# Kernel optimization log

Hardware: AMD Instinct MI355X
Metric: run time of the kernel (lower is better)

The kernel has to match this reference:

```python
import jax, jax.numpy as jnp
import numpy as np

# Module hyperparameters (from init_kwargs)
H, F = 8, 32            # num_heads, attention_filters
RY, RX = 3, 3           # spatial_radius
PH, PW = 2 * RY + 1, 2 * RX + 1
S = PH * PW             # patch_size = 49
HF = H * F


def setup_inputs() -> dict:
    key = jax.random.key(0)
    ks = jax.random.split(key, 6)
    B, Y, X, C = 4, 64, 64, 256
    x = jax.random.normal(ks[0], (B, Y, X, C), jnp.float32)
    # 1x1 conv kernels == dense matrices over the channel dim (no bias)
    Wq = jax.random.normal(ks[1], (C, HF), jnp.float32) / np.sqrt(C)
    Wk = jax.random.normal(ks[2], (C, HF), jnp.float32) / np.sqrt(C)
    Wv = jax.random.normal(ks[3], (C, HF), jnp.float32) / np.sqrt(C)
    Wo = jax.random.normal(ks[4], (HF, C), jnp.float32) / np.sqrt(HF)
    pos_emb = jax.random.normal(ks[5], (S, HF), jnp.float32) * 0.02
    return {"x": x, "Wq": Wq, "Wk": Wk, "Wv": Wv, "Wo": Wo, "pos_emb": pos_emb}


def reference(x, Wq, Wk, Wv, Wo, pos_emb):
    B, Y, X, C = x.shape
    dtype = x.dtype
    # 1x1 conv projections
    Q = x @ Wq                       # (B,Y,X,HF)
    K = x @ Wk
    V = x @ Wv
    # clipped patch centers (borders reuse interior patches)
    cy = jnp.clip(jnp.arange(Y), RY, Y - RY - 1)   # (Y,)
    cx = jnp.clip(jnp.arange(X), RX, X - RX - 1)   # (X,)
    # query relative-position indices within its patch
    qy = jnp.arange(Y) - cy + RY
    qx = jnp.arange(X) - cx + RX
    qidx = qy[:, None] * PW + qx[None, :]          # (Y,X) in [0,S)
    Q = Q + pos_emb[qidx]                          # add query pos embedding (HF)
    Q = Q.reshape(B, Y, X, H, F)
    K = K.reshape(B, Y, X, H, F)
    V = V.reshape(B, Y, X, H, F)
    cy_g, cx_g = jnp.meshgrid(cy, cx, indexing="ij")  # (Y,X)
    scale = jnp.asarray(1.0 / np.sqrt(F), dtype)
    NEG = jnp.asarray(-1e9, dtype)
    m = jnp.full((B, Y, X, H, 1), NEG, dtype)      # running max
    l = jnp.zeros((B, Y, X, H, 1), dtype)          # running sum-exp
    acc = jnp.zeros((B, Y, X, H, F), dtype)        # running value accumulator
    dy_vec = np.arange(-RY, RY + 1)                # within-chunk offsets ('col' mode)
    for dx in range(-RX, RX + 1):                  # chunk loop over columns (7 chunks)
        ny = jnp.clip(cy_g[None, :, :] + dy_vec[:, None, None], 0, Y - 1)  # (PH,Y,X)
        nx = jnp.clip(cx_g[None, :, :] + dx, 0, X - 1)                     # (1,Y,X)
        nx = jnp.broadcast_to(nx, ny.shape)
        sidx = (dy_vec + RY) * PW + (dx + RX)      # (PH,) relative-pos indices
        # gather neighbor K/V: (B,PH,Y,X,H,F)
        Kc = K[:, ny, nx] + pos_emb[sidx].reshape(PH, 1, 1, H, F)
        Vc = V[:, ny, nx]
        sc = jnp.einsum("byxhf,bsyxhf->byxhs", Q, Kc) * scale  # (B,Y,X,H,PH)
        new_m = jnp.maximum(m, sc.max(axis=-1, keepdims=True))
        alpha = jnp.exp(m - new_m)
        p = jnp.exp(sc - new_m)
        l = l * alpha + p.sum(axis=-1, keepdims=True)
        acc = acc * alpha + jnp.einsum("byxhs,bsyxhf->byxhf", p, Vc)
        m = new_m
    out = (acc / (l + 1e-8)).reshape(B, Y, X, HF) @ Wo
    return out
```

## Files before the change

kernel.cpp:

```cpp
#include <hip/hip_runtime.h>
#include <hip/hip_bf16.h>

static constexpr int NPOS = 4 * 64 * 64;
static constexpr int CD   = 256;
#define QSCALE (0.17677669529663687f * 1.4426950408889634f)

typedef __attribute__((ext_vector_type(8))) short bf16x8;
typedef __attribute__((ext_vector_type(4))) float f32x4;

__device__ __forceinline__ float bf2f(unsigned short u) {
    return __uint_as_float((unsigned int)u << 16);
}
__device__ __forceinline__ unsigned short bfbits(float f) {
    union { __hip_bfloat16 h; unsigned short u; } cv;
    cv.h = __float2bfloat16(f);
    return cv.u;
}
__device__ __forceinline__ unsigned int packbf2(float lo, float hi) {
    union { __hip_bfloat162 h; unsigned int u; } cv;
    cv.h.x = __float2bfloat16(lo);
    cv.h.y = __float2bfloat16(hi);
    return cv.u;
}
__device__ __forceinline__ uint4 pack8(float4 a, float4 b) {
    uint4 u;
    u.x = packbf2(a.x, a.y); u.y = packbf2(a.z, a.w);
    u.z = packbf2(b.x, b.y); u.w = packbf2(b.z, b.w);
    return u;
}
__device__ __forceinline__ void pl32swap(unsigned &a, unsigned &b) {
    auto r = __builtin_amdgcn_permlane32_swap(a, b, false, false);
    a = r[0]; b = r[1];
}
__device__ __forceinline__ void pl16swap(unsigned &a, unsigned &b) {
    auto r = __builtin_amdgcn_permlane16_swap(a, b, false, false);
    a = r[0]; b = r[1];
}

__global__ __launch_bounds__(256) void convert_kernel(
    const float* __restrict__ Wq, const float* __restrict__ Wk,
    const float* __restrict__ Wv, const float* __restrict__ Wo,
    const float* __restrict__ pe,
    __hip_bfloat16* __restrict__ Wfrag,
    __hip_bfloat16* __restrict__ pebf,
    __hip_bfloat16* __restrict__ Wofrag)
{
    int t = blockIdx.x * 256 + threadIdx.x;
    if (t < 24576) {
        int L = t & 63, ng = (t >> 6) & 7, s = (t >> 9) & 7, T = t >> 12;
        int mat = T >> 1;
        const float* src = (mat == 0) ? Wq : (mat == 1) ? Wk : Wv;
        int ncol  = (T & 1) * 128 + ng * 16 + (L & 15);
        int kbase = s * 32 + (L >> 4) * 8;
        __hip_bfloat16* dst = Wfrag + ((size_t)((T * 8 + s) * 8 + ng) * 64 + L) * 8;
#pragma unroll
        for (int j = 0; j < 8; ++j)
            dst[j] = __float2bfloat16(src[(kbase + j) * 256 + ncol]);
    } else if (t < 26624) {
        int u = t - 24576;
        int L = u & 63, Tn = (u >> 6) & 3, h = u >> 8;
        int s = Tn * 16 + (L & 15);
        int kbase = (L >> 4) * 8;
        __hip_bfloat16* dst = pebf + ((size_t)((h * 4 + Tn) * 64 + L)) * 8;
#pragma unroll
        for (int j = 0; j < 8; ++j) {
            float v = (s < 49) ? pe[s * 256 + h * 32 + kbase + j] * QSCALE : 0.f;
            dst[j] = __float2bfloat16(v);
        }
    } else if (t < 34816) {
        int u = t - 26624;
        int L = u & 63, ng = (u >> 6) & 7, s = (u >> 9) & 7, T = (u >> 12) & 1;
        int ncol  = T * 128 + ng * 16 + (L & 15);
        int kbase = s * 32 + (L >> 4) * 8;
        __hip_bfloat16* dst = Wofrag + ((size_t)((T * 8 + s) * 8 + ng) * 64 + L) * 8;
#pragma unroll
        for (int j = 0; j < 8; ++j)
            dst[j] = __float2bfloat16(Wo[(kbase + j) * 256 + ncol]);
    }
}

__global__ __launch_bounds__(256, 4) void qkv_mfma(
    const float* __restrict__ x,
    const __hip_bfloat16* __restrict__ Wfrag,
    const float* __restrict__ pe,
    unsigned short* __restrict__ QA,
    unsigned short* __restrict__ Kd,
    unsigned short* __restrict__ Vt)
{
    __shared__ __align__(16) unsigned short smem[256 * 68];
    short* As0 = (short*)smem;
    short* As1 = As0 + 2048;
    const int t = threadIdx.x;
    const int rowbase = blockIdx.x * 64;
    const int g = blockIdx.y;
    const int L = t & 63;
    const int wave = t >> 6;
    const int quad = L >> 4, lrow = L & 15;
    const int T = g * 2 + (wave >> 1);
    const int ngb = (wave & 1) * 4;

    f32x4 acc[4][4];
#pragma unroll
    for (int i = 0; i < 4; ++i)
#pragma unroll
        for (int j = 0; j < 4; ++j) acc[i][j] = (f32x4){0.f, 0.f, 0.f, 0.f};

    const float* xsrc = x + (size_t)(rowbase + (t >> 2)) * CD + (t & 3) * 8;
    const __hip_bfloat16* wbase = Wfrag + ((size_t)(T * 8 * 8 + ngb) * 64 + L) * 8;

    float4 f0 = ((const float4*)xsrc)[0];
    float4 f1 = ((const float4*)xsrc)[1];
    ((uint4*)As0)[t] = pack8(f0, f1);
    f0 = ((const float4*)(xsrc + 32))[0];
    f1 = ((const float4*)(xsrc + 32))[1];

    bf16x8 bfr[4];
#pragma unroll
    for (int j = 0; j < 4; ++j)
        bfr[j] = *(const bf16x8*)(wbase + (size_t)j * 64 * 8);
    __syncthreads();

#pragma unroll
    for (int s = 0; s < 8; ++s) {
        bf16x8 nbfr[4];
        if (s < 7) {
#pragma unroll
            for (int j = 0; j < 4; ++j)
                nbfr[j] = *(const bf16x8*)(wbase + (size_t)((s + 1) * 8 + j) * 64 * 8);
        }
        if (s < 7) {
            ((uint4*)((s & 1) ? As0 : As1))[t] = pack8(f0, f1);
            if (s < 6) {
                f0 = ((const float4*)(xsrc + (s + 2) * 32))[0];
                f1 = ((const float4*)(xsrc + (s + 2) * 32))[1];
            }
        }
        const short* Ab = (s & 1) ? As1 : As0;
#pragma unroll
        for (int i = 0; i < 4; ++i) {
            bf16x8 af = *(const bf16x8*)(Ab + (i * 16 + lrow) * 32 + quad * 8);
#pragma unroll
            for (int j = 0; j < 4; ++j)
                acc[i][j] = __builtin_amdgcn_mfma_f32_16x16x32_bf16(af, bfr[j], acc[i][j], 0, 0, 0);
        }
        __syncthreads();
#pragma unroll
        for (int j = 0; j < 4; ++j) bfr[j] = nbfr[j];
    }

    if (g == 0) {
#pragma unroll
        for (int i = 0; i < 4; ++i)
#pragma unroll
            for (int r = 0; r < 4; ++r) {
                int row = rowbase + i * 16 + quad * 4 + r;
                int yy = (row >> 6) & 63, xx = row & 63;
                int cy = min(max(yy, 3), 60), cx = min(max(xx, 3), 60);
                int qidx = (yy - cy + 3) * 7 + (xx - cx + 3);
#pragma unroll
                for (int j = 0; j < 4; ++j) {
                    int c = wave * 64 + j * 16 + lrow;
                    QA[(size_t)row * CD + c] = bfbits(acc[i][j][r] + pe[qidx * 256 + c]);
                }
            }
    } else if (g == 1) {
#pragma unroll
        for (int i = 0; i < 4; ++i)
#pragma unroll
            for (int r = 0; r < 4; ++r) {
                int row = rowbase + i * 16 + quad * 4 + r;
#pragma unroll
                for (int j = 0; j < 4; ++j) {
                    int c = wave * 64 + j * 16 + lrow;
                    Kd[(size_t)row * CD + c] = bfbits(acc[i][j][r] * QSCALE);
                }
            }
    } else {
        unsigned short* vt = smem;
#pragma unroll
        for (int i = 0; i < 4; ++i)
#pragma unroll
            for (int j = 0; j < 4; ++j) {
                int c = wave * 64 + j * 16 + lrow;
                int row0 = i * 16 + quad * 4;
                *(unsigned int*)&vt[c * 68 + row0] =
                    (unsigned int)bfbits(acc[i][j][0]) | ((unsigned int)bfbits(acc[i][j][1]) << 16);
                *(unsigned int*)&vt[c * 68 + row0 + 2] =
                    (unsigned int)bfbits(acc[i][j][2]) | ((unsigned int)bfbits(acc[i][j][3]) << 16);
            }
        __syncthreads();
        const int grp = t >> 4, lig = t & 15;
        const int row_off = lig * 4;
#pragma unroll
        for (int pass = 0; pass < 16; ++pass) {
            int c = pass * 16 + grp;
            *(ushort4*)(Vt + (size_t)c * 16384 + rowbase + row_off) =
                *(const ushort4*)&vt[c * 68 + row_off];
        }
    }
}

__global__ __launch_bounds__(512) void attn_oproj(
    const unsigned short* __restrict__ QA,
    const unsigned short* __restrict__ Kd,
    const unsigned short* __restrict__ Vt,
    const __hip_bfloat16* __restrict__ pebf,
    const __hip_bfloat16* __restrict__ Wofrag,
    float* __restrict__ out)
{
    __shared__ __align__(16) unsigned short qpes[8][16 * 72];
    __shared__ __align__(16) unsigned short At[16 * 264];
    const int t = threadIdx.x, w = t >> 6, L = t & 63;
    const int lrow = L & 15, quad = L >> 4;
    const int bid = blockIdx.x;
    const int tile = ((bid & 7) << 7) | (bid >> 3);
    const int pos0 = tile * 16;
    const int x0 = pos0 & 63;
    const int yy = (pos0 >> 6) & 63, bb = pos0 >> 12;
    const int cy = min(max(yy, 3), 60);
    const int h = w;

    const int kc0 = min(max(x0 - 8 + lrow, 0), 63);
    const int kc1 = min(max(x0 + 8 + lrow, 0), 63);
    const f32x4 zero = {0.f, 0.f, 0.f, 0.f};
    unsigned short* qp = qpes[w];

    const int cx = min(max(x0 + lrow, 3), 60) - x0 + 5;
    int qiA[4], qiB[4];
    float mkA[4], mkB[4];
#pragma unroll
    for (int r = 0; r < 4; ++r) {
        const int sl = quad * 4 + r;
        int dxa = sl - cx;
        qiA[r] = lrow * 72 + min(max(dxa, 0), 6);
        mkA[r] = ((unsigned)dxa <= 6u) ? 1.f : 0.f;
        int dxb = 16 + sl - cx;
        qiB[r] = lrow * 72 + min(max(dxb, 0), 6);
        mkB[r] = ((unsigned)dxb <= 6u) ? 1.f : 0.f;
    }

    const bf16x8 qa = *(const bf16x8*)(QA + (size_t)(pos0 + lrow) * 256 + h * 32 + quad * 8);

#pragma unroll
    for (int Tn = 0; Tn < 4; ++Tn) {
        bf16x8 bp = *(const bf16x8*)(pebf + ((size_t)((h * 4 + Tn) * 64 + L)) * 8);
        f32x4 c = __builtin_amdgcn_mfma_f32_16x16x32_bf16(bp, qa, zero, 0, 0, 0);
        *(unsigned int*)&qp[lrow * 72 + Tn * 16 + quad * 4]     = packbf2(c[0], c[1]);
        *(unsigned int*)&qp[lrow * 72 + Tn * 16 + quad * 4 + 2] = packbf2(c[2], c[3]);
    }
    __builtin_amdgcn_s_waitcnt(0xc07f);

    float lacc = 0.f;
    f32x4 oT0 = zero, oT1 = zero;
    int rowpos = bb * 4096 + (cy - 3) * 64;

    const size_t koff = h * 32 + quad * 8;
    const size_t voff0 = (size_t)(h * 32 + lrow) * 16384 + x0 - 8 + quad * 8;
    const size_t voff1 = (size_t)(h * 32 + 16 + lrow) * 16384 + x0 - 8 + quad * 8;
    bf16x8 bk0 = *(const bf16x8*)(Kd + (size_t)(rowpos + kc0) * 256 + koff);
    bf16x8 bk1 = *(const bf16x8*)(Kd + (size_t)(rowpos + kc1) * 256 + koff);
    bf16x8 bv0 = *(const bf16x8*)(Vt + voff0 + rowpos);
    bf16x8 bv1 = *(const bf16x8*)(Vt + voff1 + rowpos);

    int qpofs = 0;
    for (int dy = 0; dy < 7; ++dy) {
        const int rnext = rowpos + 64;
        bf16x8 nk0, nk1, nv0, nv1;
        if (dy < 6) {
            nk0 = *(const bf16x8*)(Kd + (size_t)(rnext + kc0) * 256 + koff);
            nk1 = *(const bf16x8*)(Kd + (size_t)(rnext + kc1) * 256 + koff);
            nv0 = *(const bf16x8*)(Vt + voff0 + rnext);
            nv1 = *(const bf16x8*)(Vt + voff1 + rnext);
        }
        f32x4 s0 = __builtin_amdgcn_mfma_f32_16x16x32_bf16(bk0, qa, zero, 0, 0, 0);
        f32x4 s1 = __builtin_amdgcn_mfma_f32_16x16x32_bf16(bk1, qa, zero, 0, 0, 0);
        float e00 = exp2f(s0[0] + bf2f(qp[qiA[0] + qpofs])) * mkA[0];
        float e01 = exp2f(s0[1] + bf2f(qp[qiA[1] + qpofs])) * mkA[1];
        float e02 = exp2f(s0[2] + bf2f(qp[qiA[2] + qpofs])) * mkA[2];
        float e03 = exp2f(s0[3] + bf2f(qp[qiA[3] + qpofs])) * mkA[3];
        float e10 = exp2f(s1[0] + bf2f(qp[qiB[0] + qpofs])) * mkB[0];
        float e11 = exp2f(s1[1] + bf2f(qp[qiB[1] + qpofs])) * mkB[1];
        float e12 = exp2f(s1[2] + bf2f(qp[qiB[2] + qpofs])) * mkB[2];
        float e13 = exp2f(s1[3] + bf2f(qp[qiB[3] + qpofs])) * mkB[3];
        lacc += ((e00 + e01) + (e02 + e03)) + ((e10 + e11) + (e12 + e13));

        unsigned p0 = packbf2(e00, e01), p1 = packbf2(e02, e03);
        unsigned z0 = packbf2(e10, e11), z1 = packbf2(e12, e13);
        pl32swap(p0, z0);
        pl16swap(p0, z0);
        pl32swap(p1, z1);
        pl16swap(p1, z1);
        union { unsigned u[4]; bf16x8 v; } pb;
        pb.u[0] = p0; pb.u[1] = p1; pb.u[2] = z0; pb.u[3] = z1;

        oT0 = __builtin_amdgcn_mfma_f32_16x16x32_bf16(bv0, pb.v, oT0, 0, 0, 0);
        oT1 = __builtin_amdgcn_mfma_f32_16x16x32_bf16(bv1, pb.v, oT1, 0, 0, 0);
        bk0 = nk0; bk1 = nk1; bv0 = nv0; bv1 = nv1;
        rowpos = rnext;
        qpofs += 7;
    }

    lacc += __shfl_xor(lacc, 16);
    lacc += __shfl_xor(lacc, 32);
    const float inv = 1.f / (lacc + 1e-8f);

    {
        const int base = lrow * 264 + h * 32 + quad * 4;
        *(unsigned int*)&At[base]          = packbf2(oT0[0] * inv, oT0[1] * inv);
        *(unsigned int*)&At[base + 2]      = packbf2(oT0[2] * inv, oT0[3] * inv);
        *(unsigned int*)&At[base + 16]     = packbf2(oT1[0] * inv, oT1[1] * inv);
        *(unsigned int*)&At[base + 16 + 2] = packbf2(oT1[2] * inv, oT1[3] * inv);
    }
    __syncthreads();

    const int T = w >> 2;
    const int ngb = (w & 3) * 2;
    f32x4 acc[2];
    acc[0] = zero; acc[1] = zero;

#pragma unroll
    for (int s = 0; s < 8; ++s) {
        bf16x8 bfr[2];
#pragma unroll
        for (int j = 0; j < 2; ++j)
            bfr[j] = *(const bf16x8*)(Wofrag +
                      ((size_t)((T * 8 + s) * 8 + ngb + j) * 64 + L) * 8);
        bf16x8 af = *(const bf16x8*)(At + lrow * 264 + s * 32 + quad * 8);
#pragma unroll
        for (int j = 0; j < 2; ++j)
            acc[j] = __builtin_amdgcn_mfma_f32_16x16x32_bf16(af, bfr[j], acc[j], 0, 0, 0);
    }

#pragma unroll
    for (int r = 0; r < 4; ++r) {
        int row = pos0 + quad * 4 + r;
#pragma unroll
        for (int j = 0; j < 2; ++j) {
            int c = w * 32 + j * 16 + lrow;
            out[(size_t)row * CD + c] = acc[j][r];
        }
    }
}

extern "C" void kernel_launch(void* const* d_in, const int* in_sizes, int n_in,
                              void* d_out, int out_size, void* d_ws, size_t ws_size,
                              hipStream_t stream)
{
    const float* x  = (const float*)d_in[0];
    const float* Wq = (const float*)d_in[1];
    const float* Wk = (const float*)d_in[2];
    const float* Wv = (const float*)d_in[3];
    const float* Wo = (const float*)d_in[4];
    const float* pe = (const float*)d_in[5];
    float* out = (float*)d_out;

    char* ws = (char*)d_ws;
    unsigned short* QA = (unsigned short*)ws;
    unsigned short* Kd = (unsigned short*)(ws + (8u << 20));
    unsigned short* Vt = (unsigned short*)(ws + (16u << 20));
    char* fr = ws + (24u << 20) + 4096;
    __hip_bfloat16* Wfrag  = (__hip_bfloat16*)fr;
    __hip_bfloat16* pebf   = (__hip_bfloat16*)(fr + (384u << 10));
    __hip_bfloat16* Wofrag = (__hip_bfloat16*)(fr + (416u << 10));

    convert_kernel<<<136, 256, 0, stream>>>(Wq, Wk, Wv, Wo, pe, Wfrag, pebf, Wofrag);
    qkv_mfma<<<dim3(256, 3), 256, 0, stream>>>(x, Wfrag, pe, QA, Kd, Vt);
    attn_oproj<<<1024, 512, 0, stream>>>(QA, Kd, Vt, pebf, Wofrag, out);
}
```

Measured before the change: 124.8 us.

## Merge Q/K/V projection blocks to load each x tile once into LDS

The QKV projection kernel used to launch three separate blocks per 64-row tile, one each for Q, K and V. Each of those blocks streamed the same fp32 x rows from global memory through a double-buffered LDS pipeline. Now a single 768-thread block loads the whole 64x256 x tile into LDS as bf16 once and runs twelve waves covering all three projections. This removes the threefold redundant x reads and the per-step barriers, at the cost of no overlap between the x load and the MFMA work, larger blocks, and a tighter register budget from the new launch bounds.

```diff
diff --git a/kernel.cpp b/kernel.cpp
--- a/kernel.cpp
+++ b/kernel.cpp
@@ -79,7 +79,7 @@
     }
 }
 
-__global__ __launch_bounds__(256, 4) void qkv_mfma(
+__global__ __launch_bounds__(768, 3) void qkv_mfma(
     const float* __restrict__ x,
     const __hip_bfloat16* __restrict__ Wfrag,
     const float* __restrict__ pe,
@@ -88,16 +88,25 @@
     unsigned short* __restrict__ Vt)
 {
     __shared__ __align__(16) unsigned short smem[256 * 68];
-    short* As0 = (short*)smem;
-    short* As1 = As0 + 2048;
+    unsigned short* As = smem;
     const int t = threadIdx.x;
     const int rowbase = blockIdx.x * 64;
-    const int g = blockIdx.y;
     const int L = t & 63;
-    const int wave = t >> 6;
+    const int w = t >> 6;
     const int quad = L >> 4, lrow = L & 15;
-    const int T = g * 2 + (wave >> 1);
-    const int ngb = (wave & 1) * 4;
+    const int T = w >> 1;
+    const int ngb = (w & 1) * 4;
+    const int g = T >> 1;
+    const int lw = w & 3;
+
+#pragma unroll
+    for (int idx = t; idx < 2048; idx += 768) {
+        const int row = idx >> 5, ch8 = idx & 31;
+        const float* src = x + (size_t)(rowbase + row) * CD + ch8 * 8;
+        float4 f0 = ((const float4*)src)[0];
+        float4 f1 = ((const float4*)src)[1];
+        *(uint4*)&As[row * 264 + ch8 * 8] = pack8(f0, f1);
+    }
 
     f32x4 acc[4][4];
 #pragma unroll
@@ -105,19 +114,12 @@
 #pragma unroll
         for (int j = 0; j < 4; ++j) acc[i][j] = (f32x4){0.f, 0.f, 0.f, 0.f};
 
-    const float* xsrc = x + (size_t)(rowbase + (t >> 2)) * CD + (t & 3) * 8;
-    const __hip_bfloat16* wbase = Wfrag + ((size_t)(T * 8 * 8 + ngb) * 64 + L) * 8;
-
-    float4 f0 = ((const float4*)xsrc)[0];
-    float4 f1 = ((const float4*)xsrc)[1];
-    ((uint4*)As0)[t] = pack8(f0, f1);
-    f0 = ((const float4*)(xsrc + 32))[0];
-    f1 = ((const float4*)(xsrc + 32))[1];
-
+    const __hip_bfloat16* wbase = Wfrag + ((size_t)(T * 64 + ngb) * 64 + L) * 8;
     bf16x8 bfr[4];
 #pragma unroll
     for (int j = 0; j < 4; ++j)
         bfr[j] = *(const bf16x8*)(wbase + (size_t)j * 64 * 8);
+
     __syncthreads();
 
 #pragma unroll
@@ -128,25 +130,18 @@
             for (int j = 0; j < 4; ++j)
                 nbfr[j] = *(const bf16x8*)(wbase + (size_t)((s + 1) * 8 + j) * 64 * 8);
         }
-        if (s < 7) {
-            ((uint4*)((s & 1) ? As0 : As1))[t] = pack8(f0, f1);
-            if (s < 6) {
-                f0 = ((const float4*)(xsrc + (s + 2) * 32))[0];
-                f1 = ((const float4*)(xsrc + (s + 2) * 32))[1];
-            }
-        }
-        const short* Ab = (s & 1) ? As1 : As0;
 #pragma unroll
         for (int i = 0; i < 4; ++i) {
-            bf16x8 af = *(const bf16x8*)(Ab + (i * 16 + lrow) * 32 + quad * 8);
+            bf16x8 af = *(const bf16x8*)&As[(i * 16 + lrow) * 264 + s * 32 + quad * 8];
 #pragma unroll
             for (int j = 0; j < 4; ++j)
                 acc[i][j] = __builtin_amdgcn_mfma_f32_16x16x32_bf16(af, bfr[j], acc[i][j], 0, 0, 0);
         }
-        __syncthreads();
 #pragma unroll
         for (int j = 0; j < 4; ++j) bfr[j] = nbfr[j];
     }
+
+    __syncthreads();
 
     if (g == 0) {
 #pragma unroll
@@ -159,7 +154,7 @@
                 int qidx = (yy - cy + 3) * 7 + (xx - cx + 3);
 #pragma unroll
                 for (int j = 0; j < 4; ++j) {
-                    int c = wave * 64 + j * 16 + lrow;
+                    int c = lw * 64 + j * 16 + lrow;
                     QA[(size_t)row * CD + c] = bfbits(acc[i][j][r] + pe[qidx * 256 + c]);
                 }
             }
@@ -171,7 +166,7 @@
                 int row = rowbase + i * 16 + quad * 4 + r;
 #pragma unroll
                 for (int j = 0; j < 4; ++j) {
-                    int c = wave * 64 + j * 16 + lrow;
+                    int c = lw * 64 + j * 16 + lrow;
                     Kd[(size_t)row * CD + c] = bfbits(acc[i][j][r] * QSCALE);
                 }
             }
@@ -181,16 +176,21 @@
         for (int i = 0; i < 4; ++i)
 #pragma unroll
             for (int j = 0; j < 4; ++j) {
-                int c = wave * 64 + j * 16 + lrow;
+                int c = lw * 64 + j * 16 + lrow;
                 int row0 = i * 16 + quad * 4;
                 *(unsigned int*)&vt[c * 68 + row0] =
                     (unsigned int)bfbits(acc[i][j][0]) | ((unsigned int)bfbits(acc[i][j][1]) << 16);
                 *(unsigned int*)&vt[c * 68 + row0 + 2] =
                     (unsigned int)bfbits(acc[i][j][2]) | ((unsigned int)bfbits(acc[i][j][3]) << 16);
             }
-        __syncthreads();
-        const int grp = t >> 4, lig = t & 15;
+    }
+    __syncthreads();
+
+    if (g == 2) {
+        const int t4 = t - 512;
+        const int grp = t4 >> 4, lig = t4 & 15;
         const int row_off = lig * 4;
+        unsigned short* vt = smem;
 #pragma unroll
         for (int pass = 0; pass < 16; ++pass) {
             int c = pass * 16 + grp;
@@ -364,6 +364,6 @@
     __hip_bfloat16* Wofrag = (__hip_bfloat16*)(fr + (416u << 10));
 
     convert_kernel<<<136, 256, 0, stream>>>(Wq, Wk, Wv, Wo, pe, Wfrag, pebf, Wofrag);
-    qkv_mfma<<<dim3(256, 3), 256, 0, stream>>>(x, Wfrag, pe, QA, Kd, Vt);
+    qkv_mfma<<<256, 768, 0, stream>>>(x, Wfrag, pe, QA, Kd, Vt);
     attn_oproj<<<1024, 512, 0, stream>>>(QA, Kd, Vt, pebf, Wofrag, out);
 }
```

New measurement: 125.5 us. About the same (+0.6%).
